# Kernel optimization log

Measured on AMD Instinct MI355X. Metric: run time of the kernel, lower is better.

The kernel has to match this reference:

```python
import jax, jax.numpy as jnp
import numpy as np

N_HEAD = 16
THETA = 10000.0


def _freqs_cos_sin(head_dim, seq_len):
    # matches precompute_freqs_cis: freqs = 1/theta^(arange(0,dim,2)/dim), outer with t
    inv = 1.0 / (THETA ** (jnp.arange(0, head_dim, 2, dtype=jnp.float32) / head_dim))
    t = jnp.arange(seq_len, dtype=jnp.float32)
    ang = jnp.outer(t, inv)  # [L, head_dim//2]
    return jnp.cos(ang), jnp.sin(ang)


def _rope(x, cos, sin):
    # x: [B, H, L, D]; pairs are interleaved (view_as_complex on (..., D//2, 2))
    x1 = x[..., 0::2]
    x2 = x[..., 1::2]
    out_re = x1 * cos - x2 * sin
    out_im = x1 * sin + x2 * cos
    return jnp.stack([out_re, out_im], axis=-1).reshape(x.shape)


def setup_inputs() -> dict:
    key = jax.random.key(0)
    ks = jax.random.split(key, 11)
    B, L, D = 2, 2048, 1024
    s = 0.02
    return {
        "q": jax.random.normal(ks[0], (B, L, D), jnp.float32),
        "k": jax.random.normal(ks[1], (B, L, D), jnp.float32),
        "v": jax.random.normal(ks[2], (B, L, D), jnp.float32),
        "wq": jax.random.normal(ks[3], (D, D), jnp.float32) * s,
        "bq": jax.random.normal(ks[4], (D,), jnp.float32) * s,
        "wk": jax.random.normal(ks[5], (D, D), jnp.float32) * s,
        "bk": jax.random.normal(ks[6], (D,), jnp.float32) * s,
        "wv": jax.random.normal(ks[7], (D, D), jnp.float32) * s,
        "bv": jax.random.normal(ks[8], (D,), jnp.float32) * s,
        "wo": jax.random.normal(ks[9], (D, D), jnp.float32) * s,
        "bo": jax.random.normal(ks[10], (D,), jnp.float32) * s,
    }


def reference(q, k, v, wq, bq, wk, bk, wv, bv, wo, bo):
    B, L, D = q.shape
    Hd = D // N_HEAD
    # projections (nn.Linear: x @ W^T + b)
    qp = q @ wq.T + bq
    kp = k @ wk.T + bk
    vp = v @ wv.T + bv
    # split: [B, L, D] -> [B, H, L, Hd]
    def split(t):
        return t.reshape(B, L, N_HEAD, Hd).transpose(0, 2, 1, 3)
    qh, kh, vh = split(qp), split(kp), split(vp)
    cos, sin = _freqs_cos_sin(Hd, L)  # [L, Hd//2], broadcasts over B, H
    qh = _rope(qh, cos, sin)
    kh = _rope(kh, cos, sin)
    # scaled dot-product attention (no mask)
    scores = jnp.einsum("bhqd,bhkd->bhqk", qh, kh) / jnp.sqrt(jnp.float32(Hd))
    attn = jax.nn.softmax(scores, axis=-1)
    out = jnp.einsum("bhqk,bhkd->bhqd", attn, vh)
    # concat heads and output projection
    out = out.transpose(0, 2, 1, 3).reshape(B, L, D)
    return out @ wo.T + bo
```

## Files before the change

### kernel.cpp

```cpp
#include <hip/hip_runtime.h>
#include <hip/hip_bf16.h>
#include <math.h>

#define BB 2
#define LL 2048
#define DD 1024
#define NH 16
#define HD 64

typedef short v8s __attribute__((ext_vector_type(8)));
typedef float v4f __attribute__((ext_vector_type(4)));
typedef float v16f __attribute__((ext_vector_type(16)));

__device__ __forceinline__ float b2f(unsigned short b) {
  union { unsigned int u; float f; } c; c.u = ((unsigned int)b) << 16; return c.f;
}
__device__ __forceinline__ unsigned short f2b(float x) {
  union { float f; unsigned int u; } c; c.f = x;
  unsigned int u = c.u;
  u += 0x7fffu + ((u >> 16) & 1u);
  return (unsigned short)(u >> 16);
}
__device__ __forceinline__ unsigned int asu(float x) {
  union { float f; unsigned int u; } c; c.f = x; return c.u;
}
__device__ __forceinline__ unsigned int pk2(float lo, float hi) {
  return __builtin_amdgcn_perm(asu(hi), asu(lo), 0x07060302u);
}

#if defined(__has_builtin)
#if __has_builtin(__builtin_amdgcn_exp2f)
#define EXP2(x) __builtin_amdgcn_exp2f(x)
#else
#define EXP2(x) __expf((x) * 0.69314718056f)
#endif
#else
#define EXP2(x) __expf((x) * 0.69314718056f)
#endif

__device__ __forceinline__ void gload16(const void* g, void* l) {
  __builtin_amdgcn_global_load_lds(
      (const __attribute__((address_space(1))) void*)g,
      (__attribute__((address_space(3))) void*)l, 16, 0, 0);
}

struct CastArgs { const float* s[7]; unsigned short* d[7]; float* ct; float* st; };
__global__ void cast_all(CastArgs a) {
  int z = blockIdx.z;
  if (z == 16) {
    if (blockIdx.x >= 256) return;
    int id = blockIdx.x * blockDim.x + threadIdx.x;
    int t = id >> 5, i = id & 31;
    float inv = powf(10000.0f, -(float)(2 * i) / 64.0f);
    float ang = (float)t * inv;
    a.ct[id] = cosf(ang);
    a.st[id] = sinf(ang);
    return;
  }
  int t = (z < 12) ? (z >> 2) : (z - 9);
  int off = (z < 12) ? ((z & 3) << 18) : 0;
  int i = off + blockIdx.x * blockDim.x + threadIdx.x;
  float4 v = ((const float4*)a.s[t])[i];
  ushort4 o;
  o.x = f2b(v.x); o.y = f2b(v.y); o.z = f2b(v.z); o.w = f2b(v.w);
  ((ushort4*)a.d[t])[i] = o;
}

template <typename OutT>
__device__ __forceinline__ void gemm_body(const unsigned short* __restrict__ X,
                                          const unsigned short* __restrict__ W,
                                          const float* __restrict__ bias,
                                          OutT* __restrict__ Y,
                                          int M, int N, int K) {
  __shared__ __align__(16) unsigned short As[128 * 64];
  __shared__ __align__(16) unsigned short Bs[128 * 64];
  const int tid = threadIdx.x;
  const int lane = tid & 63, wave = tid >> 6;
  const int quad = lane >> 4, l16 = lane & 15;
  const int bn0 = blockIdx.x * 128;
  const int bm0 = blockIdx.y * 128;
  const int wm = (wave >> 1) * 64, wn = (wave & 1) * 64;

  const v4f vzero = {0.f, 0.f, 0.f, 0.f};
  v4f acc[4][4];
#pragma unroll
  for (int i = 0; i < 4; ++i)
#pragma unroll
    for (int j = 0; j < 4; ++j) acc[i][j] = vzero;

  for (int k0 = 0; k0 < K; k0 += 64) {
#pragma unroll
    for (int c = 0; c < 4; ++c) {
      int id = c * 256 + tid;
      int r = id >> 3, cc = ((id & 7) ^ (r & 7)) * 8;
      gload16(X + (size_t)(bm0 + r) * K + k0 + cc, &As[id * 8]);
    }
#pragma unroll
    for (int c = 0; c < 4; ++c) {
      int id = c * 256 + tid;
      int r = id >> 3, cc = ((id & 7) ^ (r & 7)) * 8;
      gload16(W + (size_t)(bn0 + r) * K + k0 + cc, &Bs[id * 8]);
    }
    __syncthreads();
#pragma unroll
    for (int kh = 0; kh < 2; ++kh) {
      v8s a[4], b[4];
#pragma unroll
      for (int i = 0; i < 4; ++i) {
        int ra = wm + i * 16 + l16;
        int sa = (kh * 4 + quad) ^ (ra & 7);
        a[i] = *(const v8s*)&As[ra * 64 + sa * 8];
        int rb = wn + i * 16 + l16;
        int sb = (kh * 4 + quad) ^ (rb & 7);
        b[i] = *(const v8s*)&Bs[rb * 64 + sb * 8];
      }
#pragma unroll
      for (int mi = 0; mi < 4; ++mi)
#pragma unroll
        for (int ni = 0; ni < 4; ++ni)
          acc[mi][ni] = __builtin_amdgcn_mfma_f32_16x16x32_bf16(a[mi], b[ni], acc[mi][ni], 0, 0, 0);
    }
    __syncthreads();
  }

  float bv[4];
#pragma unroll
  for (int ni = 0; ni < 4; ++ni) bv[ni] = bias[bn0 + wn + ni * 16 + l16];
#pragma unroll
  for (int mi = 0; mi < 4; ++mi) {
#pragma unroll
    for (int r = 0; r < 4; ++r) {
      int row = bm0 + wm + mi * 16 + quad * 4 + r;
      size_t base = (size_t)row * N + bn0 + wn + l16;
#pragma unroll
      for (int ni = 0; ni < 4; ++ni) {
        float v = acc[mi][ni][r] + bv[ni];
        if constexpr (sizeof(OutT) == 2) {
          Y[base + ni * 16] = (OutT)f2b(v);
        } else {
          Y[base + ni * 16] = (OutT)v;
        }
      }
    }
  }
}

__global__ __launch_bounds__(256) void gemm_qkv(
    const unsigned short* x0, const unsigned short* w0, const float* b0, unsigned short* y0,
    const unsigned short* x1, const unsigned short* w1, const float* b1, unsigned short* y1,
    const unsigned short* x2, const unsigned short* w2, const float* b2, unsigned short* y2) {
  const unsigned short *X, *W; const float* Bp; unsigned short* Y;
  if (blockIdx.z == 0)      { X = x0; W = w0; Bp = b0; Y = y0; }
  else if (blockIdx.z == 1) { X = x1; W = w1; Bp = b1; Y = y1; }
  else                      { X = x2; W = w2; Bp = b2; Y = y2; }
  gemm_body<unsigned short>(X, W, Bp, Y, BB * LL, DD, DD);
}

__global__ __launch_bounds__(256) void gemm_out(
    const unsigned short* x, const unsigned short* w, const float* b, float* y) {
  gemm_body<float>(x, w, b, y, BB * LL, DD, DD);
}

__global__ void prep_kernel(const unsigned short* __restrict__ qp,
                            const unsigned short* __restrict__ kp,
                            const unsigned short* __restrict__ vp,
                            unsigned short* __restrict__ qh,
                            unsigned short* __restrict__ kh,
                            unsigned short* __restrict__ vt,
                            const float* __restrict__ ctab,
                            const float* __restrict__ stab) {
  if (blockIdx.z < 2) {
    int id = blockIdx.x * blockDim.x + threadIdx.x;
    const unsigned short* src = (blockIdx.z == 0) ? qp : kp;
    unsigned short* dst = (blockIdx.z == 0) ? qh : kh;
    float sc = (blockIdx.z == 0) ? 0.18033688f : 1.0f;
    int i = id & 31;
    int l = (id >> 5) & (LL - 1);
    int h = (id >> 16) & (NH - 1);
    int b = id >> 20;
    ushort2 v = ((const ushort2*)(src + ((size_t)(b * LL + l) * DD + h * HD)))[i];
    float c = ctab[l * 32 + i], s = stab[l * 32 + i];
    float x1 = b2f(v.x), x2 = b2f(v.y);
    ushort2 o;
    o.x = f2b((x1 * c - x2 * s) * sc);
    o.y = f2b((x1 * s + x2 * c) * sc);
    ((ushort2*)(dst + (size_t)((b * NH + h) * LL + l) * HD))[i] = o;
    return;
  }
  if (blockIdx.x >= 1024) return;
  __shared__ unsigned short T[64][65];
  int bh = blockIdx.x >> 5;
  int b = bh >> 4, h = bh & 15;
  int l0 = (blockIdx.x & 31) * 64;
  int t = threadIdx.x;
  int lr = t >> 2, seg = (t & 3) * 16;
  const unsigned short* src = vp + ((size_t)(b * LL + l0 + lr) * DD + h * HD + seg);
  ushort4 u0 = ((const ushort4*)src)[0];
  ushort4 u1 = ((const ushort4*)src)[1];
  ushort4 u2 = ((const ushort4*)src)[2];
  ushort4 u3 = ((const ushort4*)src)[3];
  T[lr][seg + 0] = u0.x;  T[lr][seg + 1] = u0.y;  T[lr][seg + 2] = u0.z;  T[lr][seg + 3] = u0.w;
  T[lr][seg + 4] = u1.x;  T[lr][seg + 5] = u1.y;  T[lr][seg + 6] = u1.z;  T[lr][seg + 7] = u1.w;
  T[lr][seg + 8] = u2.x;  T[lr][seg + 9] = u2.y;  T[lr][seg + 10] = u2.z; T[lr][seg + 11] = u2.w;
  T[lr][seg + 12] = u3.x; T[lr][seg + 13] = u3.y; T[lr][seg + 14] = u3.z; T[lr][seg + 15] = u3.w;
  __syncthreads();
  int dr = t >> 2, ls = (t & 3) * 16;
  unsigned short* dst = vt + ((size_t)(bh * HD + dr) * LL + l0 + ls);
  ushort4 o0, o1, o2, o3;
  o0.x = T[ls + 0][dr];  o0.y = T[ls + 1][dr];  o0.z = T[ls + 2][dr];  o0.w = T[ls + 3][dr];
  o1.x = T[ls + 4][dr];  o1.y = T[ls + 5][dr];  o1.z = T[ls + 6][dr];  o1.w = T[ls + 7][dr];
  o2.x = T[ls + 8][dr];  o2.y = T[ls + 9][dr];  o2.z = T[ls + 10][dr]; o2.w = T[ls + 11][dr];
  o3.x = T[ls + 12][dr]; o3.y = T[ls + 13][dr]; o3.z = T[ls + 14][dr]; o3.w = T[ls + 15][dr];
  ((ushort4*)dst)[0] = o0; ((ushort4*)dst)[2] = o1;
  ((ushort4*)dst)[1] = o2; ((ushort4*)dst)[3] = o3;
}

__global__ __launch_bounds__(256, 4) void flash_kernel(
    const unsigned short* __restrict__ qh,
    const unsigned short* __restrict__ kh,
    const unsigned short* __restrict__ vt,
    unsigned short* __restrict__ attn) {
  __shared__ __align__(16) unsigned short S_[128 * 64 + 64 * 128];
  unsigned short* Ks = S_;
  unsigned short* Vs = S_ + 128 * 64;
  const int tid = threadIdx.x, wave = tid >> 6, lane = tid & 63;
  const int l32 = lane & 31, hf = lane >> 5;
  const int bh = blockIdx.y, b = bh >> 4, hd = bh & 15;
  const int q0 = blockIdx.x * 128;
  const unsigned short* qbase = qh + (size_t)bh * LL * HD;
  const unsigned short* kbase = kh + (size_t)bh * LL * HD;
  const unsigned short* vbase = vt + (size_t)bh * HD * LL;

  const int qrow = q0 + wave * 32 + l32;
  v8s qf[4];
#pragma unroll
  for (int ks2 = 0; ks2 < 4; ++ks2)
    qf[ks2] = *(const v8s*)(qbase + (size_t)qrow * HD + ks2 * 16 + hf * 8);

  v16f o0, o1;
#pragma unroll
  for (int i = 0; i < 16; ++i) { o0[i] = 0.0f; o1[i] = 0.0f; }
  float ls = 0.0f;

  for (int kt = 0; kt < LL; kt += 128) {
#pragma unroll
    for (int i = 0; i < 4; ++i) {
      int id = i * 256 + tid;
      int r = id >> 3, c = (id & 7) ^ (r & 7);
      gload16(kbase + (size_t)(kt + r) * HD + c * 8, &Ks[id * 8]);
    }
#pragma unroll
    for (int i = 0; i < 4; ++i) {
      int id = i * 256 + tid;
      int r = id >> 4, c = (id & 15) ^ (r & 15);
      gload16(vbase + (size_t)r * LL + kt + c * 8, &Vs[id * 8]);
    }
    __syncthreads();

#pragma unroll
    for (int g = 0; g < 4; ++g) {
      v16f sc;
#pragma unroll
      for (int i = 0; i < 16; ++i) sc[i] = 0.0f;
#pragma unroll
      for (int ks2 = 0; ks2 < 4; ++ks2) {
        int row = g * 32 + l32;
        int slot = (ks2 * 2 + hf) ^ (lane & 7);
        v8s kf = *(const v8s*)&Ks[row * 64 + slot * 8];
        sc = __builtin_amdgcn_mfma_f32_32x32x16_bf16(kf, qf[ks2], sc, 0, 0, 0);
      }
      v16f e;
#pragma unroll
      for (int i = 0; i < 16; ++i) e[i] = EXP2(sc[i]);
      float t0 = (e[0] + e[1]) + (e[2] + e[3]);
      float t1 = (e[4] + e[5]) + (e[6] + e[7]);
      float t2 = (e[8] + e[9]) + (e[10] + e[11]);
      float t3 = (e[12] + e[13]) + (e[14] + e[15]);
      ls += (t0 + t1) + (t2 + t3);
#pragma unroll
      for (int k2 = 0; k2 < 2; ++k2) {
        union { v8s v; unsigned int u[4]; } pb;
#pragma unroll
        for (int a = 0; a < 4; ++a)
          pb.u[a] = pk2(e[8 * k2 + 2 * a], e[8 * k2 + 2 * a + 1]);
        int k16 = g * 2 + k2;
        int slotv = (k16 * 2 + hf) ^ (lane & 15);
        v8s vf0 = *(const v8s*)&Vs[l32 * 128 + slotv * 8];
        v8s vf1 = *(const v8s*)&Vs[(32 + l32) * 128 + slotv * 8];
        o0 = __builtin_amdgcn_mfma_f32_32x32x16_bf16(vf0, pb.v, o0, 0, 0, 0);
        o1 = __builtin_amdgcn_mfma_f32_32x32x16_bf16(vf1, pb.v, o1, 0, 0, 0);
      }
    }
    __syncthreads();
  }

  ls += __shfl_xor(ls, 32);
  float inv = 1.0f / ls;

  unsigned short* Wt = &Ks[wave * 2048];
#pragma unroll
  for (int dt = 0; dt < 2; ++dt)
#pragma unroll
    for (int r = 0; r < 16; ++r) {
      int dl = (r & 3) + 8 * (r >> 2) + 4 * hf;
      int d = dt * 32 + dl;
      int chunk = d >> 3, offw = d & 7;
      int slot = chunk ^ (l32 & 7);
      float val = (dt == 0) ? o0[r] : o1[r];
      Wt[l32 * 64 + slot * 8 + offw] = f2b(val * inv);
    }
#pragma unroll
  for (int i = 0; i < 4; ++i) {
    int qr = lane >> 1;
    int chunk = (lane & 1) * 4 + i;
    int slot = chunk ^ (qr & 7);
    v8s dv = *(const v8s*)&Wt[qr * 64 + slot * 8];
    int token = q0 + wave * 32 + qr;
    *(v8s*)(attn + ((size_t)(b * LL + token) * DD) + hd * HD + chunk * 8) = dv;
  }
}

extern "C" void kernel_launch(void* const* d_in, const int* in_sizes, int n_in,
                              void* d_out, int out_size, void* d_ws, size_t ws_size,
                              hipStream_t stream) {
  const float* q  = (const float*)d_in[0];
  const float* k  = (const float*)d_in[1];
  const float* v  = (const float*)d_in[2];
  const float* wq = (const float*)d_in[3];
  const float* bq = (const float*)d_in[4];
  const float* wk = (const float*)d_in[5];
  const float* bk = (const float*)d_in[6];
  const float* wv = (const float*)d_in[7];
  const float* bv = (const float*)d_in[8];
  const float* wo = (const float*)d_in[9];
  const float* bo = (const float*)d_in[10];
  float* out = (float*)d_out;

  size_t off = 0;
  char* wsb = (char*)d_ws;
  auto take = [&](size_t n) { void* p = wsb + off; off += n; return p; };
  const size_t SZT = (size_t)BB * LL * DD * 2;
  const size_t SZW = (size_t)DD * DD * 2;
  unsigned short* qb   = (unsigned short*)take(SZT);
  unsigned short* kb   = (unsigned short*)take(SZT);
  unsigned short* vb   = (unsigned short*)take(SZT);
  unsigned short* wqb  = (unsigned short*)take(SZW);
  unsigned short* wkb  = (unsigned short*)take(SZW);
  unsigned short* wvb  = (unsigned short*)take(SZW);
  unsigned short* wob  = (unsigned short*)take(SZW);
  unsigned short* qp   = (unsigned short*)take(SZT);
  unsigned short* kp   = (unsigned short*)take(SZT);
  unsigned short* vp   = (unsigned short*)take(SZT);
  unsigned short* qhh  = (unsigned short*)take(SZT);
  unsigned short* khh  = (unsigned short*)take(SZT);
  unsigned short* vtt  = (unsigned short*)take(SZT);
  unsigned short* attn = (unsigned short*)take(SZT);
  float* ctab = (float*)take((size_t)LL * 32 * 4);
  float* stab = (float*)take((size_t)LL * 32 * 4);

  CastArgs ca;
  ca.s[0] = q;  ca.s[1] = k;  ca.s[2] = v;  ca.s[3] = wq;
  ca.s[4] = wk; ca.s[5] = wv; ca.s[6] = wo;
  ca.d[0] = qb;  ca.d[1] = kb;  ca.d[2] = vb;  ca.d[3] = wqb;
  ca.d[4] = wkb; ca.d[5] = wvb; ca.d[6] = wob;
  ca.ct = ctab; ca.st = stab;
  cast_all<<<dim3(1024, 1, 17), 256, 0, stream>>>(ca);

  gemm_qkv<<<dim3(DD / 128, BB * LL / 128, 3), 256, 0, stream>>>(
      qb, wqb, bq, qp, kb, wkb, bk, kp, vb, wvb, bv, vp);

  prep_kernel<<<dim3((BB * NH * LL * 32) / 256, 1, 3), 256, 0, stream>>>(
      qp, kp, vp, qhh, khh, vtt, ctab, stab);

  flash_kernel<<<dim3(LL / 128, BB * NH), 256, 0, stream>>>(qhh, khh, vtt, attn);

  gemm_out<<<dim3(DD / 128, BB * LL / 128, 1), 256, 0, stream>>>(attn, wob, bo, out);
}
```

Measured before the change: 243.1 us.

## Fuse V transpose into QKV GEMM, Q RoPE into flash, double-buffer K/V

The QKV GEMM now writes V directly in transposed per-head layout through an LDS staging pass, which removes the separate V transpose. Q RoPE and softmax scaling move into the flash kernel's Q fragment load, so the prep pass shrinks to a K-only RoPE kernel. The flash kernel double-buffers K/V tiles in 64KB of LDS so the next tile's global loads overlap the current tile's compute, with one barrier per iteration. Doubling the LDS per block lowers launch bounds occupancy from 4 to 2 blocks per CU.

```diff
diff --git a/kernel.cpp b/kernel.cpp
--- a/kernel.cpp
+++ b/kernel.cpp
@@ -146,14 +146,116 @@
 }
 
 __global__ __launch_bounds__(256) void gemm_qkv(
-    const unsigned short* x0, const unsigned short* w0, const float* b0, unsigned short* y0,
-    const unsigned short* x1, const unsigned short* w1, const float* b1, unsigned short* y1,
-    const unsigned short* x2, const unsigned short* w2, const float* b2, unsigned short* y2) {
-  const unsigned short *X, *W; const float* Bp; unsigned short* Y;
-  if (blockIdx.z == 0)      { X = x0; W = w0; Bp = b0; Y = y0; }
-  else if (blockIdx.z == 1) { X = x1; W = w1; Bp = b1; Y = y1; }
-  else                      { X = x2; W = w2; Bp = b2; Y = y2; }
-  gemm_body<unsigned short>(X, W, Bp, Y, BB * LL, DD, DD);
+    const unsigned short* __restrict__ qb, const unsigned short* __restrict__ kb,
+    const unsigned short* __restrict__ vb,
+    const unsigned short* __restrict__ wqb, const unsigned short* __restrict__ wkb,
+    const unsigned short* __restrict__ wvb,
+    const float* __restrict__ bq, const float* __restrict__ bk,
+    const float* __restrict__ bv_,
+    unsigned short* __restrict__ qp, unsigned short* __restrict__ kp,
+    unsigned short* __restrict__ vt) {
+  __shared__ __align__(16) unsigned short LDS_[16384];
+  unsigned short* As = LDS_;
+  unsigned short* Bs = LDS_ + 8192;
+  const int z = blockIdx.z;
+  const unsigned short* X = (z == 0) ? qb : (z == 1) ? kb : vb;
+  const unsigned short* W = (z == 0) ? wqb : (z == 1) ? wkb : wvb;
+  const float* bias = (z == 0) ? bq : (z == 1) ? bk : bv_;
+  const int K = DD, N = DD;
+  const int tid = threadIdx.x;
+  const int lane = tid & 63, wave = tid >> 6;
+  const int quad = lane >> 4, l16 = lane & 15;
+  const int bn0 = blockIdx.x * 128;
+  const int bm0 = blockIdx.y * 128;
+  const int wm = (wave >> 1) * 64, wn = (wave & 1) * 64;
+
+  const v4f vzero = {0.f, 0.f, 0.f, 0.f};
+  v4f acc[4][4];
+#pragma unroll
+  for (int i = 0; i < 4; ++i)
+#pragma unroll
+    for (int j = 0; j < 4; ++j) acc[i][j] = vzero;
+
+  for (int k0 = 0; k0 < K; k0 += 64) {
+#pragma unroll
+    for (int c = 0; c < 4; ++c) {
+      int id = c * 256 + tid;
+      int r = id >> 3, cc = ((id & 7) ^ (r & 7)) * 8;
+      gload16(X + (size_t)(bm0 + r) * K + k0 + cc, &As[id * 8]);
+    }
+#pragma unroll
+    for (int c = 0; c < 4; ++c) {
+      int id = c * 256 + tid;
+      int r = id >> 3, cc = ((id & 7) ^ (r & 7)) * 8;
+      gload16(W + (size_t)(bn0 + r) * K + k0 + cc, &Bs[id * 8]);
+    }
+    __syncthreads();
+#pragma unroll
+    for (int kh = 0; kh < 2; ++kh) {
+      v8s a[4], b[4];
+#pragma unroll
+      for (int i = 0; i < 4; ++i) {
+        int ra = wm + i * 16 + l16;
+        int sa = (kh * 4 + quad) ^ (ra & 7);
+        a[i] = *(const v8s*)&As[ra * 64 + sa * 8];
+        int rb = wn + i * 16 + l16;
+        int sb = (kh * 4 + quad) ^ (rb & 7);
+        b[i] = *(const v8s*)&Bs[rb * 64 + sb * 8];
+      }
+#pragma unroll
+      for (int mi = 0; mi < 4; ++mi)
+#pragma unroll
+        for (int ni = 0; ni < 4; ++ni)
+          acc[mi][ni] = __builtin_amdgcn_mfma_f32_16x16x32_bf16(a[mi], b[ni], acc[mi][ni], 0, 0, 0);
+    }
+    __syncthreads();
+  }
+
+  float bv[4];
+#pragma unroll
+  for (int ni = 0; ni < 4; ++ni) bv[ni] = bias[bn0 + wn + ni * 16 + l16];
+
+  if (z < 2) {
+    unsigned short* Y = (z == 0) ? qp : kp;
+#pragma unroll
+    for (int mi = 0; mi < 4; ++mi)
+#pragma unroll
+      for (int r = 0; r < 4; ++r) {
+        int row = bm0 + wm + mi * 16 + quad * 4 + r;
+        size_t base = (size_t)row * N + bn0 + wn + l16;
+#pragma unroll
+        for (int ni = 0; ni < 4; ++ni)
+          Y[base + ni * 16] = f2b(acc[mi][ni][r] + bv[ni]);
+      }
+  } else {
+#pragma unroll
+    for (int mi = 0; mi < 4; ++mi)
+#pragma unroll
+      for (int r = 0; r < 4; ++r) {
+        int tl = wm + mi * 16 + quad * 4 + r;
+        int tlp = (tl & ~12) | ((tl & 4) << 1) | ((tl & 8) >> 1);
+        int chunk = tlp >> 3, offw = tlp & 7;
+#pragma unroll
+        for (int ni = 0; ni < 4; ++ni) {
+          int fl = wn + ni * 16 + l16;
+          LDS_[fl * 128 + ((chunk ^ (fl & 15)) * 8) + offw] =
+              f2b(acc[mi][ni][r] + bv[ni]);
+        }
+      }
+    __syncthreads();
+    int fl = tid >> 1, half = tid & 1;
+    int fg = bn0 + fl;
+    int h = fg >> 6, d = fg & 63;
+    int bidx = bm0 >> 11, l0 = bm0 & (LL - 1);
+    unsigned short* dst =
+        vt + (((size_t)(bidx * NH + h) * HD + d) * LL) + l0 + half * 64;
+#pragma unroll
+    for (int i = 0; i < 8; ++i) {
+      int chunk = half * 8 + i;
+      int slot = chunk ^ (fl & 15);
+      *(v8s*)(dst + i * 8) = *(const v8s*)&LDS_[fl * 128 + slot * 8];
+    }
+  }
 }
 
 __global__ __launch_bounds__(256) void gemm_out(
@@ -161,101 +263,106 @@
   gemm_body<float>(x, w, b, y, BB * LL, DD, DD);
 }
 
-__global__ void prep_kernel(const unsigned short* __restrict__ qp,
-                            const unsigned short* __restrict__ kp,
-                            const unsigned short* __restrict__ vp,
-                            unsigned short* __restrict__ qh,
-                            unsigned short* __restrict__ kh,
-                            unsigned short* __restrict__ vt,
-                            const float* __restrict__ ctab,
-                            const float* __restrict__ stab) {
-  if (blockIdx.z < 2) {
-    int id = blockIdx.x * blockDim.x + threadIdx.x;
-    const unsigned short* src = (blockIdx.z == 0) ? qp : kp;
-    unsigned short* dst = (blockIdx.z == 0) ? qh : kh;
-    float sc = (blockIdx.z == 0) ? 0.18033688f : 1.0f;
-    int i = id & 31;
-    int l = (id >> 5) & (LL - 1);
-    int h = (id >> 16) & (NH - 1);
-    int b = id >> 20;
-    ushort2 v = ((const ushort2*)(src + ((size_t)(b * LL + l) * DD + h * HD)))[i];
-    float c = ctab[l * 32 + i], s = stab[l * 32 + i];
-    float x1 = b2f(v.x), x2 = b2f(v.y);
-    ushort2 o;
-    o.x = f2b((x1 * c - x2 * s) * sc);
-    o.y = f2b((x1 * s + x2 * c) * sc);
-    ((ushort2*)(dst + (size_t)((b * NH + h) * LL + l) * HD))[i] = o;
-    return;
-  }
-  if (blockIdx.x >= 1024) return;
-  __shared__ unsigned short T[64][65];
-  int bh = blockIdx.x >> 5;
-  int b = bh >> 4, h = bh & 15;
-  int l0 = (blockIdx.x & 31) * 64;
-  int t = threadIdx.x;
-  int lr = t >> 2, seg = (t & 3) * 16;
-  const unsigned short* src = vp + ((size_t)(b * LL + l0 + lr) * DD + h * HD + seg);
-  ushort4 u0 = ((const ushort4*)src)[0];
-  ushort4 u1 = ((const ushort4*)src)[1];
-  ushort4 u2 = ((const ushort4*)src)[2];
-  ushort4 u3 = ((const ushort4*)src)[3];
-  T[lr][seg + 0] = u0.x;  T[lr][seg + 1] = u0.y;  T[lr][seg + 2] = u0.z;  T[lr][seg + 3] = u0.w;
-  T[lr][seg + 4] = u1.x;  T[lr][seg + 5] = u1.y;  T[lr][seg + 6] = u1.z;  T[lr][seg + 7] = u1.w;
-  T[lr][seg + 8] = u2.x;  T[lr][seg + 9] = u2.y;  T[lr][seg + 10] = u2.z; T[lr][seg + 11] = u2.w;
-  T[lr][seg + 12] = u3.x; T[lr][seg + 13] = u3.y; T[lr][seg + 14] = u3.z; T[lr][seg + 15] = u3.w;
-  __syncthreads();
-  int dr = t >> 2, ls = (t & 3) * 16;
-  unsigned short* dst = vt + ((size_t)(bh * HD + dr) * LL + l0 + ls);
-  ushort4 o0, o1, o2, o3;
-  o0.x = T[ls + 0][dr];  o0.y = T[ls + 1][dr];  o0.z = T[ls + 2][dr];  o0.w = T[ls + 3][dr];
-  o1.x = T[ls + 4][dr];  o1.y = T[ls + 5][dr];  o1.z = T[ls + 6][dr];  o1.w = T[ls + 7][dr];
-  o2.x = T[ls + 8][dr];  o2.y = T[ls + 9][dr];  o2.z = T[ls + 10][dr]; o2.w = T[ls + 11][dr];
-  o3.x = T[ls + 12][dr]; o3.y = T[ls + 13][dr]; o3.z = T[ls + 14][dr]; o3.w = T[ls + 15][dr];
-  ((ushort4*)dst)[0] = o0; ((ushort4*)dst)[2] = o1;
-  ((ushort4*)dst)[1] = o2; ((ushort4*)dst)[3] = o3;
-}
-
-__global__ __launch_bounds__(256, 4) void flash_kernel(
-    const unsigned short* __restrict__ qh,
+__global__ void ropek_kernel(const unsigned short* __restrict__ kp,
+                             unsigned short* __restrict__ kh,
+                             const float* __restrict__ ctab,
+                             const float* __restrict__ stab) {
+  int id = blockIdx.x * blockDim.x + threadIdx.x;
+  int i = id & 31;
+  int l = (id >> 5) & (LL - 1);
+  int h = (id >> 16) & (NH - 1);
+  int b = id >> 20;
+  ushort2 v = ((const ushort2*)(kp + ((size_t)(b * LL + l) * DD + h * HD)))[i];
+  float c = ctab[l * 32 + i], s = stab[l * 32 + i];
+  float x1 = b2f(v.x), x2 = b2f(v.y);
+  ushort2 o;
+  o.x = f2b(x1 * c - x2 * s);
+  o.y = f2b(x1 * s + x2 * c);
+  ((ushort2*)(kh + (size_t)((b * NH + h) * LL + l) * HD))[i] = o;
+}
+
+__global__ __launch_bounds__(256, 2) void flash_kernel(
+    const unsigned short* __restrict__ qp,
     const unsigned short* __restrict__ kh,
     const unsigned short* __restrict__ vt,
-    unsigned short* __restrict__ attn) {
-  __shared__ __align__(16) unsigned short S_[128 * 64 + 64 * 128];
-  unsigned short* Ks = S_;
-  unsigned short* Vs = S_ + 128 * 64;
+    unsigned short* __restrict__ attn,
+    const float* __restrict__ ctab, const float* __restrict__ stab) {
+  __shared__ __align__(16) unsigned short S_[2][16384];
   const int tid = threadIdx.x, wave = tid >> 6, lane = tid & 63;
   const int l32 = lane & 31, hf = lane >> 5;
   const int bh = blockIdx.y, b = bh >> 4, hd = bh & 15;
   const int q0 = blockIdx.x * 128;
-  const unsigned short* qbase = qh + (size_t)bh * LL * HD;
   const unsigned short* kbase = kh + (size_t)bh * LL * HD;
   const unsigned short* vbase = vt + (size_t)bh * HD * LL;
 
   const int qrow = q0 + wave * 32 + l32;
   v8s qf[4];
-#pragma unroll
-  for (int ks2 = 0; ks2 < 4; ++ks2)
-    qf[ks2] = *(const v8s*)(qbase + (size_t)qrow * HD + ks2 * 16 + hf * 8);
+  {
+    const float scq = 0.18033688f;
+    const unsigned short* qsrc = qp + ((size_t)(b * LL + qrow) * DD + hd * HD);
+#pragma unroll
+    for (int ks2 = 0; ks2 < 4; ++ks2) {
+      union { v8s v; unsigned int u[4]; } raw, outp;
+      raw.v = *(const v8s*)(qsrc + ks2 * 16 + hf * 8);
+      float4 c4 = ((const float4*)ctab)[qrow * 8 + ks2 * 2 + hf];
+      float4 s4 = ((const float4*)stab)[qrow * 8 + ks2 * 2 + hf];
+      float cs[4] = {c4.x, c4.y, c4.z, c4.w};
+      float ss[4] = {s4.x, s4.y, s4.z, s4.w};
+#pragma unroll
+      for (int j = 0; j < 4; ++j) {
+        float x1 = b2f((unsigned short)(raw.u[j] & 0xffff));
+        float x2 = b2f((unsigned short)(raw.u[j] >> 16));
+        float o0 = (x1 * cs[j] - x2 * ss[j]) * scq;
+        float o1 = (x1 * ss[j] + x2 * cs[j]) * scq;
+        outp.u[j] = (unsigned int)f2b(o0) | ((unsigned int)f2b(o1) << 16);
+      }
+      qf[ks2] = outp.v;
+    }
+  }
 
   v16f o0, o1;
 #pragma unroll
   for (int i = 0; i < 16; ++i) { o0[i] = 0.0f; o1[i] = 0.0f; }
   float ls = 0.0f;
 
-  for (int kt = 0; kt < LL; kt += 128) {
+  {
+    unsigned short* Kb = S_[0];
+    unsigned short* Vb = S_[0] + 8192;
 #pragma unroll
     for (int i = 0; i < 4; ++i) {
       int id = i * 256 + tid;
       int r = id >> 3, c = (id & 7) ^ (r & 7);
-      gload16(kbase + (size_t)(kt + r) * HD + c * 8, &Ks[id * 8]);
+      gload16(kbase + (size_t)r * HD + c * 8, &Kb[id * 8]);
     }
 #pragma unroll
     for (int i = 0; i < 4; ++i) {
       int id = i * 256 + tid;
       int r = id >> 4, c = (id & 15) ^ (r & 15);
-      gload16(vbase + (size_t)r * LL + kt + c * 8, &Vs[id * 8]);
-    }
-    __syncthreads();
+      gload16(vbase + (size_t)r * LL + c * 8, &Vb[id * 8]);
+    }
+  }
+
+  for (int t = 0; t < 16; ++t) {
+    __syncthreads();
+    if (t < 15) {
+      int kt = (t + 1) * 128;
+      unsigned short* Kb = S_[(t + 1) & 1];
+      unsigned short* Vb = Kb + 8192;
+#pragma unroll
+      for (int i = 0; i < 4; ++i) {
+        int id = i * 256 + tid;
+        int r = id >> 3, c = (id & 7) ^ (r & 7);
+        gload16(kbase + (size_t)(kt + r) * HD + c * 8, &Kb[id * 8]);
+      }
+#pragma unroll
+      for (int i = 0; i < 4; ++i) {
+        int id = i * 256 + tid;
+        int r = id >> 4, c = (id & 15) ^ (r & 15);
+        gload16(vbase + (size_t)r * LL + kt + c * 8, &Vb[id * 8]);
+      }
+    }
+    const unsigned short* Ks = S_[t & 1];
+    const unsigned short* Vs = Ks + 8192;
 
 #pragma unroll
     for (int g = 0; g < 4; ++g) {
@@ -291,13 +398,12 @@
         o1 = __builtin_amdgcn_mfma_f32_32x32x16_bf16(vf1, pb.v, o1, 0, 0, 0);
       }
     }
-    __syncthreads();
   }
 
   ls += __shfl_xor(ls, 32);
   float inv = 1.0f / ls;
 
-  unsigned short* Wt = &Ks[wave * 2048];
+  unsigned short* Wt = S_[0] + wave * 2048;
 #pragma unroll
   for (int dt = 0; dt < 2; ++dt)
 #pragma unroll
@@ -350,8 +456,6 @@
   unsigned short* wob  = (unsigned short*)take(SZW);
   unsigned short* qp   = (unsigned short*)take(SZT);
   unsigned short* kp   = (unsigned short*)take(SZT);
-  unsigned short* vp   = (unsigned short*)take(SZT);
-  unsigned short* qhh  = (unsigned short*)take(SZT);
   unsigned short* khh  = (unsigned short*)take(SZT);
   unsigned short* vtt  = (unsigned short*)take(SZT);
   unsigned short* attn = (unsigned short*)take(SZT);
@@ -367,12 +471,12 @@
   cast_all<<<dim3(1024, 1, 17), 256, 0, stream>>>(ca);
 
   gemm_qkv<<<dim3(DD / 128, BB * LL / 128, 3), 256, 0, stream>>>(
-      qb, wqb, bq, qp, kb, wkb, bk, kp, vb, wvb, bv, vp);
-
-  prep_kernel<<<dim3((BB * NH * LL * 32) / 256, 1, 3), 256, 0, stream>>>(
-      qp, kp, vp, qhh, khh, vtt, ctab, stab);
-
-  flash_kernel<<<dim3(LL / 128, BB * NH), 256, 0, stream>>>(qhh, khh, vtt, attn);
+      qb, kb, vb, wqb, wkb, wvb, bq, bk, bv, qp, kp, vtt);
+
+  ropek_kernel<<<(BB * NH * LL * 32) / 256, 256, 0, stream>>>(kp, khh, ctab, stab);
+
+  flash_kernel<<<dim3(LL / 128, BB * NH), 256, 0, stream>>>(
+      qp, khh, vtt, attn, ctab, stab);
 
   gemm_out<<<dim3(DD / 128, BB * LL / 128, 1), 256, 0, stream>>>(attn, wob, bo, out);
 }
```

Result: faster. 236.6 us (-2.7%).
